# Optimization experiments

Hardware: AMD Instinct MI355X
Metric: run time of the kernel (lower is better)

## Reference

```python
import jax, jax.numpy as jnp
import numpy as np
from jax import lax

B, L, D_MODEL = 2, 1024, 768
N_LAYER, D_STATE, D_CONV, EXPAND = 8, 16, 4, 2
D_INNER = EXPAND * D_MODEL          # 1536
DT_RANK = -(-D_MODEL // 16)         # 48 (MambaConfig 'auto')


def setup_inputs() -> dict:
    key = jax.random.key(0)
    ks = jax.random.split(key, 10)
    s = 0.02
    batch = jax.random.normal(ks[0], (B, D_MODEL, L), jnp.float32)
    lengths = jax.random.randint(ks[1], (B,), L // 2, L + 1)
    mask = jnp.arange(L)[None, :] < lengths[:, None]          # valid-prefix mask [B,L]
    norm_w = jnp.ones((N_LAYER, D_MODEL), jnp.float32)
    W_in = jax.random.normal(ks[2], (N_LAYER, 2 * D_INNER, D_MODEL), jnp.float32) * s
    conv_w = jax.random.normal(ks[3], (N_LAYER, D_INNER, D_CONV), jnp.float32) * 0.5
    conv_b = jnp.zeros((N_LAYER, D_INNER), jnp.float32)
    W_x = jax.random.normal(ks[4], (N_LAYER, DT_RANK + 2 * D_STATE, D_INNER), jnp.float32) * s
    W_dt = jax.random.normal(ks[5], (N_LAYER, D_INNER, DT_RANK), jnp.float32) * (DT_RANK ** -0.5)
    # mamba dt init: dt ~ logU[1e-3, 0.1], bias = softplus^-1(dt)
    dt = jnp.exp(jax.random.uniform(ks[6], (N_LAYER, D_INNER)) * (np.log(0.1) - np.log(1e-3)) + np.log(1e-3))
    b_dt = jnp.log(jnp.expm1(dt)).astype(jnp.float32)
    A_log = jnp.log(jnp.broadcast_to(jnp.arange(1, D_STATE + 1, dtype=jnp.float32), (N_LAYER, D_INNER, D_STATE))).copy()
    D_skip = jnp.ones((N_LAYER, D_INNER), jnp.float32)
    W_out = jax.random.normal(ks[7], (N_LAYER, D_MODEL, D_INNER), jnp.float32) * s
    normf_w = jnp.ones((D_MODEL,), jnp.float32)
    return dict(batch=batch, mask=mask, norm_w=norm_w, W_in=W_in, conv_w=conv_w, conv_b=conv_b,
                W_x=W_x, W_dt=W_dt, b_dt=b_dt, A_log=A_log, D_skip=D_skip, W_out=W_out, normf_w=normf_w)


def _rmsnorm(x, w, eps=1e-5):
    return x * w * lax.rsqrt(jnp.mean(x * x, axis=-1, keepdims=True) + eps)


def _mamba(x, W_in, cw, cb, W_x, W_dt, b_dt, A_log, Dsk, W_out):
    Bb, Ls, _ = x.shape
    d_inner, d_conv = cw.shape
    d_state = A_log.shape[-1]
    dt_rank = W_dt.shape[-1]
    xz = jnp.einsum('bld,ed->ble', x, W_in)                    # [B,L,2*d_inner]
    xc, z = jnp.split(xz, 2, axis=-1)
    # causal depthwise conv1d (+bias) then SiLU
    xt = lax.conv_general_dilated(xc.transpose(0, 2, 1), cw[:, None, :], (1,),
                                  [(d_conv - 1, 0)], feature_group_count=d_inner)
    u = jax.nn.silu(xt + cb[None, :, None]).transpose(0, 2, 1)  # [B,L,d_inner]
    dbl = jnp.einsum('bld,ed->ble', u, W_x)
    dtp, Bm, Cm = jnp.split(dbl, [dt_rank, dt_rank + d_state], axis=-1)
    delta = jax.nn.softplus(jnp.einsum('blr,dr->bld', dtp, W_dt) + b_dt)  # [B,L,d_inner]
    A = -jnp.exp(A_log)                                         # [d_inner,d_state]

    def step(h, t):
        d_t, b_t, c_t, u_t = t                                  # [B,di],[B,ds],[B,ds],[B,di]
        h = jnp.exp(d_t[..., None] * A) * h + (d_t * u_t)[..., None] * b_t[:, None, :]
        return h, jnp.einsum('bds,bs->bd', h, c_t)

    h0 = jnp.zeros((Bb, d_inner, d_state), x.dtype)
    _, ys = lax.scan(step, h0, (delta.transpose(1, 0, 2), Bm.transpose(1, 0, 2),
                                Cm.transpose(1, 0, 2), u.transpose(1, 0, 2)))
    y = ys.transpose(1, 0, 2) + u * Dsk
    return jnp.einsum('bld,ed->ble', y * jax.nn.silu(z), W_out)


def _forward(batch, mask, norm_w, W_in, conv_w, conv_b, W_x, W_dt, b_dt, A_log, D_skip, W_out, normf_w):
    h = jnp.transpose(batch, (0, 2, 1))                         # [B,L,D]
    for i in range(norm_w.shape[0]):                            # pre-norm residual blocks
        h = h + _mamba(_rmsnorm(h, norm_w[i]), W_in[i], conv_w[i], conv_b[i],
                       W_x[i], W_dt[i], b_dt[i], A_log[i], D_skip[i], W_out[i])
    h = _rmsnorm(h, normf_w)
    # last valid token: first False of mask (or L if none), minus 1
    inv = ~mask
    lengths = jnp.where(jnp.any(inv, axis=1), jnp.argmax(inv, axis=1), mask.shape[1]) - 1
    return jnp.take_along_axis(h, lengths[:, None, None], axis=1)[:, 0, :]


def reference(batch, mask, norm_w, W_in, conv_w, conv_b, W_x, W_dt, b_dt, A_log, D_skip, W_out, normf_w):
    return _forward(batch, mask, norm_w, W_in, conv_w, conv_b, W_x, W_dt, b_dt, A_log, D_skip, W_out, normf_w)
```

## Files before the change

### kernel.cpp

```cpp
#include <hip/hip_runtime.h>
#include <hip/hip_bf16.h>
#include <math.h>

#define BB 2
#define LL 1024
#define DM 768
#define NL 8
#define DS 16
#define DC 4
#define DI 1536
#define DTR 48
#define NTOK (BB*LL)
#define WXROWS (DTR + 2*DS)
#define NC 64
#define CT (LL/NC)
#define SKS 8
#define SKC (DI/SKS)
#define SK4 3
#define SK4C (DI/SK4)
#define DTB 8
#define RBLK 128

typedef __attribute__((ext_vector_type(8))) short bf16x8;
typedef __attribute__((ext_vector_type(4))) float f32x4;

__device__ inline void gload_lds16(const void* g, void* l) {
    __builtin_amdgcn_global_load_lds(
        (const __attribute__((address_space(1))) unsigned int*)g,
        (__attribute__((address_space(3))) unsigned int*)l, 16, 0, 0);
}

__device__ inline int xcd_swz(int orig, int nwg) {
    return (orig & 7) * (nwg >> 3) + (orig >> 3);
}

__device__ inline void gemm_core64(
    const __hip_bfloat16* __restrict__ gA0,
    const __hip_bfloat16* __restrict__ gW0, const __hip_bfloat16* __restrict__ gW1,
    int kbeg, int kend, int w, int wr, int wc, int fr, int khi,
    f32x4 (&acc)[2][4])
{
    __shared__ short As[2048];
    __shared__ short Ws[4096];
    short* AsW = As + w * 512;
    short* WsW = Ws + w * 512;
    for (int k0 = kbeg; k0 < kend; k0 += 32) {
        gload_lds16(gA0 + k0, AsW);
        gload_lds16(gW0 + k0, WsW);
        gload_lds16(gW1 + k0, WsW + 2048);
        asm volatile("s_waitcnt vmcnt(0)" ::: "memory");
        __syncthreads();
        bf16x8 a4[2], b4[4];
        #pragma unroll
        for (int mi = 0; mi < 2; ++mi)
            a4[mi] = *(const bf16x8*)&As[(wr*32 + mi*16 + fr)*32 + khi*8];
        #pragma unroll
        for (int ni = 0; ni < 4; ++ni)
            b4[ni] = *(const bf16x8*)&Ws[(wc*64 + ni*16 + fr)*32 + khi*8];
        #pragma unroll
        for (int mi = 0; mi < 2; ++mi)
            #pragma unroll
            for (int ni = 0; ni < 4; ++ni)
                acc[mi][ni] = __builtin_amdgcn_mfma_f32_16x16x32_bf16(
                    a4[mi], b4[ni], acc[mi][ni], 0, 0, 0);
        __syncthreads();
    }
}

__global__ __launch_bounds__(256) void transpose_in_kernel(
    const float* __restrict__ batch, float* __restrict__ h)
{
    __shared__ float tile[32][33];
    const int b  = blockIdx.z;
    const int l0 = blockIdx.x * 32;
    const int d0 = blockIdx.y * 32;
    const int tx = threadIdx.x & 31;
    const int ty = threadIdx.x >> 5;
    #pragma unroll
    for (int i = ty; i < 32; i += 8)
        tile[i][tx] = batch[((size_t)b*DM + d0 + i)*LL + l0 + tx];
    __syncthreads();
    #pragma unroll
    for (int i = ty; i < 32; i += 8)
        h[((size_t)b*LL + l0 + i)*DM + d0 + tx] = tile[tx][i];
}

__global__ void lengths_kernel(const void* __restrict__ mask, int* __restrict__ lengths)
{
    int b = threadIdx.x;
    if (b >= BB) return;
    const unsigned int* mi = (const unsigned int*)mask;
    bool packed = (mi[0] == 0x01010101u);
    int cnt = 0;
    if (packed) {
        const unsigned char* mb = (const unsigned char*)mask;
        for (int i = 0; i < LL; ++i) cnt += (mb[(size_t)b*LL + i] != 0);
    } else {
        for (int i = 0; i < LL; ++i) cnt += (mi[(size_t)b*LL + i] != 0);
    }
    lengths[b] = cnt;
}

__global__ __launch_bounds__(256) void cvt_bf16_kernel(
    const float* __restrict__ in, __hip_bfloat16* __restrict__ o, int n)
{
    int i = (blockIdx.x * 256 + threadIdx.x) * 4;
    if (i >= n) return;
    float4 v = *(const float4*)(in + i);
    __hip_bfloat16 h0 = __float2bfloat16(v.x);
    __hip_bfloat16 h1 = __float2bfloat16(v.y);
    __hip_bfloat16 h2 = __float2bfloat16(v.z);
    __hip_bfloat16 h3 = __float2bfloat16(v.w);
    ushort4 r;
    r.x = *(unsigned short*)&h0; r.y = *(unsigned short*)&h1;
    r.z = *(unsigned short*)&h2; r.w = *(unsigned short*)&h3;
    *(ushort4*)(o + i) = r;
}

__global__ __launch_bounds__(256) void cvt_padrow_kernel(
    const float* __restrict__ in, __hip_bfloat16* __restrict__ o,
    int nrin, int nrout, int ncol, int nmat)
{
    int i = (blockIdx.x * 256 + threadIdx.x) * 4;
    int tot = nmat * nrout * ncol;
    if (i >= tot) return;
    int m = i / (nrout * ncol);
    int rem = i - m * (nrout * ncol);
    int r = rem / ncol;
    int c = rem - r * ncol;
    ushort4 rr = {0,0,0,0};
    if (r < nrin) {
        float4 v = *(const float4*)(in + ((size_t)m*nrin + r)*ncol + c);
        __hip_bfloat16 h0 = __float2bfloat16(v.x);
        __hip_bfloat16 h1 = __float2bfloat16(v.y);
        __hip_bfloat16 h2 = __float2bfloat16(v.z);
        __hip_bfloat16 h3 = __float2bfloat16(v.w);
        rr.x = *(unsigned short*)&h0; rr.y = *(unsigned short*)&h1;
        rr.z = *(unsigned short*)&h2; rr.w = *(unsigned short*)&h3;
    }
    *(ushort4*)(o + i) = rr;
}

__global__ __launch_bounds__(256) void rmsnorm_kernel(
    const float* __restrict__ x, const float* __restrict__ w,
    __hip_bfloat16* __restrict__ o)
{
    int tok = blockIdx.x;
    const float* xr = x + (size_t)tok * DM;
    float ss = 0.f;
    for (int j = threadIdx.x; j < DM; j += 256) { float v = xr[j]; ss += v*v; }
    #pragma unroll
    for (int off = 32; off > 0; off >>= 1) ss += __shfl_down(ss, off);
    __shared__ float red[4];
    int lane = threadIdx.x & 63, wv = threadIdx.x >> 6;
    if (lane == 0) red[wv] = ss;
    __syncthreads();
    if (threadIdx.x == 0) {
        float t = red[0] + red[1] + red[2] + red[3];
        red[0] = rsqrtf(t / (float)DM + 1e-5f);
    }
    __syncthreads();
    float r = red[0];
    for (int j = threadIdx.x; j < DM; j += 256)
        o[(size_t)tok*DM + j] = __float2bfloat16(xr[j] * w[j] * r);
}

__global__ __launch_bounds__(256) void gemm_mfma_kernel(
    const __hip_bfloat16* __restrict__ A,
    const __hip_bfloat16* __restrict__ W,
    __hip_bfloat16* __restrict__ C,
    int NT, int M, int N, int K)
{
    const int swz = xcd_swz(blockIdx.x, gridDim.x);
    const int bn = (swz % NT) * 128;
    const int bm = (swz / NT) * 64;
    const int t = threadIdx.x;
    const int w = t >> 6;
    const int lane = t & 63;
    const int wr = w >> 1, wc = w & 1;
    const int fr = lane & 15;
    const int khi = lane >> 4;

    f32x4 acc[2][4];
    #pragma unroll
    for (int mi = 0; mi < 2; ++mi)
        #pragma unroll
        for (int ni = 0; ni < 4; ++ni)
            acc[mi][ni] = (f32x4){0.f, 0.f, 0.f, 0.f};

    const int rowL = t >> 2;
    const int ks = (t & 3) * 8;
    gemm_core64(A + (size_t)(bm + rowL) * K + ks,
                W + (size_t)(bn + rowL) * K + ks,
                W + (size_t)(bn + 64 + rowL) * K + ks,
                0, K, w, wr, wc, fr, khi, acc);

    #pragma unroll
    for (int mi = 0; mi < 2; ++mi) {
        #pragma unroll
        for (int ni = 0; ni < 4; ++ni) {
            int gc = bn + wc*64 + ni*16 + fr;
            #pragma unroll
            for (int r = 0; r < 4; ++r) {
                int gr = bm + wr*32 + mi*16 + khi*4 + r;
                C[(size_t)gr * N + gc] = __float2bfloat16(acc[mi][ni][r]);
            }
        }
    }
}

__global__ __launch_bounds__(256) void gemm_mfma_splitk4(
    const __hip_bfloat16* __restrict__ A,
    const __hip_bfloat16* __restrict__ W,
    float* __restrict__ Cp)
{
    const int swz = xcd_swz(blockIdx.x, gridDim.x);
    const int bm = (swz / 18) * 64;
    const int r18 = swz % 18;
    const int bn = (r18 % 6) * 128;
    const int split = r18 / 6;
    const int t = threadIdx.x;
    const int w = t >> 6;
    const int lane = t & 63;
    const int wr = w >> 1, wc = w & 1;
    const int fr = lane & 15;
    const int khi = lane >> 4;

    f32x4 acc[2][4];
    #pragma unroll
    for (int mi = 0; mi < 2; ++mi)
        #pragma unroll
        for (int ni = 0; ni < 4; ++ni)
            acc[mi][ni] = (f32x4){0.f, 0.f, 0.f, 0.f};

    const int rowL = t >> 2;
    const int ks = (t & 3) * 8;
    const int kbeg = split * SK4C;
    gemm_core64(A + (size_t)(bm + rowL) * DI + ks,
                W + (size_t)(bn + rowL) * DI + ks,
                W + (size_t)(bn + 64 + rowL) * DI + ks,
                kbeg, kbeg + SK4C, w, wr, wc, fr, khi, acc);

    #pragma unroll
    for (int mi = 0; mi < 2; ++mi) {
        #pragma unroll
        for (int ni = 0; ni < 4; ++ni) {
            int gc = bn + wc*64 + ni*16 + fr;
            #pragma unroll
            for (int r = 0; r < 4; ++r) {
                int gr = bm + wr*32 + mi*16 + khi*4 + r;
                Cp[((size_t)split*NTOK + gr)*DM + gc] = acc[mi][ni][r];
            }
        }
    }
}

__global__ __launch_bounds__(256) void reduce_add_norm_kernel(
    const float* __restrict__ Cp, float* __restrict__ h,
    const float* __restrict__ nw, __hip_bfloat16* __restrict__ xn)
{
    int tok = blockIdx.x;
    int tid = threadIdx.x;
    float v[3];
    float ss = 0.f;
    #pragma unroll
    for (int r = 0; r < 3; ++r) {
        int j = tid + r*256;
        size_t o = (size_t)tok*DM + j;
        float x = h[o] + Cp[o] + Cp[(size_t)NTOK*DM + o] + Cp[2*(size_t)NTOK*DM + o];
        h[o] = x;
        v[r] = x;
        ss += x*x;
    }
    if (!nw) return;
    #pragma unroll
    for (int off = 32; off > 0; off >>= 1) ss += __shfl_down(ss, off);
    __shared__ float red[4];
    int lane = tid & 63, wv = tid >> 6;
    if (lane == 0) red[wv] = ss;
    __syncthreads();
    if (tid == 0) {
        float t = red[0] + red[1] + red[2] + red[3];
        red[0] = rsqrtf(t / (float)DM + 1e-5f);
    }
    __syncthreads();
    float rinv = red[0];
    #pragma unroll
    for (int r = 0; r < 3; ++r) {
        int j = tid + r*256;
        xn[(size_t)tok*DM + j] = __float2bfloat16(v[r] * nw[j] * rinv);
    }
}

__global__ __launch_bounds__(256) void gemm_mfma_skinny(
    const __hip_bfloat16* __restrict__ A,
    const __hip_bfloat16* __restrict__ W,
    float* __restrict__ Cp)
{
    const int split = blockIdx.x;
    const int bm = blockIdx.y * 64;
    const int t = threadIdx.x;
    const int w = t >> 6;
    const int lane = t & 63;
    const int wr = w >> 1, wc = w & 1;
    const int fr = lane & 15;
    const int khi = lane >> 4;

    f32x4 acc[2][4];
    #pragma unroll
    for (int mi = 0; mi < 2; ++mi)
        #pragma unroll
        for (int ni = 0; ni < 4; ++ni)
            acc[mi][ni] = (f32x4){0.f, 0.f, 0.f, 0.f};

    const int rowL = t >> 2;
    const int ks = (t & 3) * 8;
    const int kbeg = split * SKC;
    gemm_core64(A + (size_t)(bm + rowL) * DI + ks,
                W + (size_t)rowL * DI + ks,
                W + (size_t)(64 + rowL) * DI + ks,
                kbeg, kbeg + SKC, w, wr, wc, fr, khi, acc);

    #pragma unroll
    for (int mi = 0; mi < 2; ++mi) {
        #pragma unroll
        for (int ni = 0; ni < 4; ++ni) {
            int gc = wc*64 + ni*16 + fr;
            if (gc >= WXROWS) continue;
            #pragma unroll
            for (int r = 0; r < 4; ++r) {
                int gr = bm + wr*32 + mi*16 + khi*4 + r;
                Cp[((size_t)split*NTOK + gr)*WXROWS + gc] = acc[mi][ni][r];
            }
        }
    }
}

__global__ __launch_bounds__(256) void reduce_delta_kernel(
    const float* __restrict__ Cp,
    const float* __restrict__ W_dt, const float* __restrict__ b_dt,
    float* __restrict__ dbl, __hip_bfloat16* __restrict__ delta)
{
    __shared__ float ld[DTB*DTR];
    const int tid = threadIdx.x;
    const int d = blockIdx.x * 256 + tid;
    const int t0 = blockIdx.y * DTB;
    for (int j = tid; j < DTB*DTR; j += 256) {
        int tt = j / DTR, jj = j - tt*DTR;
        float s = 0.f;
        #pragma unroll
        for (int p = 0; p < SKS; ++p)
            s += Cp[((size_t)p*NTOK + t0 + tt)*WXROWS + jj];
        ld[j] = s;
    }
    if (blockIdx.x == 0) {
        for (int j = tid; j < DTB*WXROWS; j += 256) {
            int tt = j / WXROWS, jj = j - tt*WXROWS;
            float s = 0.f;
            #pragma unroll
            for (int p = 0; p < SKS; ++p)
                s += Cp[((size_t)p*NTOK + t0 + tt)*WXROWS + jj];
            dbl[(size_t)(t0 + tt)*WXROWS + jj] = s;
        }
    }
    float wdt[DTR];
    #pragma unroll
    for (int j = 0; j < DTR; j += 4) {
        float4 v = *(const float4*)(W_dt + (size_t)d*DTR + j);
        wdt[j] = v.x; wdt[j+1] = v.y; wdt[j+2] = v.z; wdt[j+3] = v.w;
    }
    const float bdt = b_dt[d];
    __syncthreads();
    #pragma unroll
    for (int tt = 0; tt < DTB; ++tt) {
        float dt = bdt;
        #pragma unroll
        for (int j = 0; j < DTR; ++j) dt = fmaf(ld[tt*DTR + j], wdt[j], dt);
        dt = (dt > 20.f) ? dt : log1pf(__expf(dt));
        delta[(size_t)(t0 + tt)*DI + d] = __float2bfloat16(dt);
    }
}

__global__ __launch_bounds__(256) void conv_silu_kernel(
    const __hip_bfloat16* __restrict__ xz, const float* __restrict__ cw,
    const float* __restrict__ cb, __hip_bfloat16* __restrict__ u)
{
    int idx = blockIdx.x * 256 + threadIdx.x;
    if (idx >= NTOK*DI/8) return;
    const int dg  = idx % (DI/8);
    const int row = idx / (DI/8);
    const int l   = row % LL;
    const int d0  = dg * 8;

    float acc[8];
    {
        float4 c0 = *(const float4*)(cb + d0);
        float4 c1 = *(const float4*)(cb + d0 + 4);
        acc[0]=c0.x; acc[1]=c0.y; acc[2]=c0.z; acc[3]=c0.w;
        acc[4]=c1.x; acc[5]=c1.y; acc[6]=c1.z; acc[7]=c1.w;
    }
    float4 cwj[8];
    #pragma unroll
    for (int j = 0; j < 8; ++j)
        cwj[j] = *(const float4*)(cw + (size_t)(d0 + j)*4);

    #pragma unroll
    for (int k = 0; k < 4; ++k) {
        int ls = l - 3 + k;
        if (ls < 0) continue;
        bf16x8 v = *(const bf16x8*)(xz + (size_t)(row - 3 + k)*(2*DI) + d0);
        const __hip_bfloat16* vp = (const __hip_bfloat16*)&v;
        #pragma unroll
        for (int j = 0; j < 8; ++j) {
            float xv = __bfloat162float(vp[j]);
            float wv = (k == 0) ? cwj[j].x : (k == 1) ? cwj[j].y : (k == 2) ? cwj[j].z : cwj[j].w;
            acc[j] = fmaf(xv, wv, acc[j]);
        }
    }
    bf16x8 r;
    __hip_bfloat16* rp = (__hip_bfloat16*)&r;
    #pragma unroll
    for (int j = 0; j < 8; ++j) {
        float s = acc[j] / (1.f + __expf(-acc[j]));
        rp[j] = __float2bfloat16(s);
    }
    *(bf16x8*)(u + (size_t)row*DI + d0) = r;
}

__global__ __launch_bounds__(256) void scan_phaseA(
    const __hip_bfloat16* __restrict__ delta, const __hip_bfloat16* __restrict__ u,
    const float* __restrict__ dbl, const float* __restrict__ A_log,
    __hip_bfloat16* __restrict__ Psum, __hip_bfloat16* __restrict__ Hsum)
{
    const int d = blockIdx.x * 256 + threadIdx.x;
    const int c = blockIdx.y;
    const int b = blockIdx.z;
    float A[DS], P[DS], hl[DS];
    #pragma unroll
    for (int s = 0; s < DS; ++s) {
        A[s] = -expf(A_log[(size_t)d*DS + s]);
        P[s] = 1.f; hl[s] = 0.f;
    }
    const int t0 = c * CT;
    for (int t = t0; t < t0 + CT; ++t) {
        const size_t row = (size_t)b*LL + t;
        const float* bc = dbl + row*WXROWS + DTR;
        float dt = __bfloat162float(delta[row*DI + d]);
        float du = dt * __bfloat162float(u[row*DI + d]);
        #pragma unroll
        for (int s = 0; s < DS; ++s) {
            float a = __expf(dt * A[s]);
            P[s] *= a;
            hl[s] = fmaf(a, hl[s], du * bc[s]);
        }
    }
    const size_t off = (((size_t)b*NC + c)*DI + d)*DS;
    #pragma unroll
    for (int s = 0; s < DS; ++s) {
        Psum[off+s] = __float2bfloat16(P[s]);
        Hsum[off+s] = __float2bfloat16(hl[s]);
    }
}

__global__ __launch_bounds__(256) void scan_phaseB(
    const __hip_bfloat16* __restrict__ Psum, const __hip_bfloat16* __restrict__ Hsum,
    __hip_bfloat16* __restrict__ Hin)
{
    __shared__ float pA[NC][RBLK];
    __shared__ float hA[NC][RBLK];
    const int tid = threadIdx.x;
    const int blk = blockIdx.x;
    const int b = blk / (DI*DS/RBLK);
    const int r0 = (blk % (DI*DS/RBLK)) * RBLK;
    for (int j = tid; j < NC*RBLK; j += 256) {
        int c = j >> 7, rr = j & (RBLK-1);
        size_t off = ((size_t)(b*NC + c))*DI*DS + r0 + rr;
        pA[c][rr] = __bfloat162float(Psum[off]);
        hA[c][rr] = __bfloat162float(Hsum[off]);
    }
    __syncthreads();
    if (tid < RBLK) {
        float hc = 0.f;
        for (int c = 0; c < NC; ++c) {
            size_t off = ((size_t)(b*NC + c))*DI*DS + r0 + tid;
            Hin[off] = __float2bfloat16(hc);
            hc = fmaf(pA[c][tid], hc, hA[c][tid]);
        }
    }
}

__global__ __launch_bounds__(256) void scan_phaseC(
    const __hip_bfloat16* __restrict__ delta, const __hip_bfloat16* __restrict__ u,
    const float* __restrict__ dbl, const __hip_bfloat16* __restrict__ xz,
    const float* __restrict__ A_log, const float* __restrict__ Dsk,
    const __hip_bfloat16* __restrict__ Hin, __hip_bfloat16* __restrict__ yfull)
{
    const int d = blockIdx.x * 256 + threadIdx.x;
    const int c = blockIdx.y;
    const int b = blockIdx.z;
    float A[DS], h[DS];
    const size_t hoff = (((size_t)b*NC + c)*DI + d)*DS;
    #pragma unroll
    for (int s = 0; s < DS; ++s) {
        A[s] = -expf(A_log[(size_t)d*DS + s]);
        h[s] = __bfloat162float(Hin[hoff + s]);
    }
    const float dsk = Dsk[d];
    const int t0 = c * CT;
    for (int t = t0; t < t0 + CT; ++t) {
        const size_t row = (size_t)b*LL + t;
        const float* bc = dbl + row*WXROWS + DTR;
        float dt = __bfloat162float(delta[row*DI + d]);
        float ut = __bfloat162float(u[row*DI + d]);
        float du = dt * ut;
        float y = 0.f;
        #pragma unroll
        for (int s = 0; s < DS; ++s) {
            float a = __expf(dt * A[s]);
            h[s] = fmaf(a, h[s], du * bc[s]);
            y = fmaf(h[s], bc[DS+s], y);
        }
        float zt = __bfloat162float(xz[row*(2*DI) + DI + d]);
        float sz = zt / (1.f + __expf(-zt));
        yfull[row*DI + d] = __float2bfloat16((y + ut * dsk) * sz);
    }
}

__global__ __launch_bounds__(256) void final_kernel(
    const float* __restrict__ h, const float* __restrict__ w,
    const int* __restrict__ lengths, float* __restrict__ out)
{
    int b = blockIdx.x;
    int idx = lengths[b] - 1;
    const float* xr = h + ((size_t)b*LL + idx)*DM;
    float ss = 0.f;
    for (int j = threadIdx.x; j < DM; j += 256) { float v = xr[j]; ss += v*v; }
    #pragma unroll
    for (int off = 32; off > 0; off >>= 1) ss += __shfl_down(ss, off);
    __shared__ float red[4];
    int lane = threadIdx.x & 63, wv = threadIdx.x >> 6;
    if (lane == 0) red[wv] = ss;
    __syncthreads();
    if (threadIdx.x == 0) {
        float t = red[0] + red[1] + red[2] + red[3];
        red[0] = rsqrtf(t / (float)DM + 1e-5f);
    }
    __syncthreads();
    float r = red[0];
    for (int j = threadIdx.x; j < DM; j += 256)
        out[(size_t)b*DM + j] = xr[j] * w[j] * r;
}

extern "C" void kernel_launch(void* const* d_in, const int* in_sizes, int n_in,
                              void* d_out, int out_size, void* d_ws, size_t ws_size,
                              hipStream_t stream)
{
    const float* batch   = (const float*)d_in[0];
    const void*  mask    = d_in[1];
    const float* norm_w  = (const float*)d_in[2];
    const float* W_in    = (const float*)d_in[3];
    const float* conv_w  = (const float*)d_in[4];
    const float* conv_b  = (const float*)d_in[5];
    const float* W_x     = (const float*)d_in[6];
    const float* W_dt    = (const float*)d_in[7];
    const float* b_dt    = (const float*)d_in[8];
    const float* A_log   = (const float*)d_in[9];
    const float* D_skip  = (const float*)d_in[10];
    const float* W_out   = (const float*)d_in[11];
    const float* normf_w = (const float*)d_in[12];
    float* out = (float*)d_out;

    float* ws   = (float*)d_ws;
    float* h    = ws;
    float* dbl  = h   + (size_t)NTOK*DM;
    float* scr  = dbl + (size_t)NTOK*WXROWS;
    const size_t SEG = (size_t)BB*NC*DI*DS;
    float* dblp = scr;
    float* Cp4  = scr;
    __hip_bfloat16* Psum = (__hip_bfloat16*)scr;
    __hip_bfloat16* Hsum = Psum + SEG;
    __hip_bfloat16* Hin  = Hsum + SEG;
    __hip_bfloat16* xz_bf    = (__hip_bfloat16*)(scr + 3*SEG);
    __hip_bfloat16* xn_bf    = xz_bf + (size_t)NTOK*2*DI;
    __hip_bfloat16* u_bf     = xn_bf + (size_t)NTOK*DM;
    __hip_bfloat16* delta_bf = u_bf  + (size_t)NTOK*DI;
    __hip_bfloat16* y_bf     = delta_bf + (size_t)NTOK*DI;
    __hip_bfloat16* wbase    = y_bf + (size_t)NTOK*DI;

    const size_t WIN_L  = (size_t)2*DI*DM;
    const size_t WOUT_L = (size_t)DM*DI;
    const size_t WXP_L  = (size_t)128*DI;
    const size_t WSUM   = WIN_L + WOUT_L + WXP_L;

    size_t need_all = (size_t)((char*)(wbase + (size_t)NL*WSUM) - (char*)d_ws) + 256;
    const bool all = ws_size >= need_all;
    const int nlw = all ? NL : 1;

    __hip_bfloat16* Win_b  = wbase;
    __hip_bfloat16* Wout_b = Win_b  + (size_t)nlw*WIN_L;
    __hip_bfloat16* Wxp_b  = Wout_b + (size_t)nlw*WOUT_L;
    int* lengths = (int*)(Wxp_b + (size_t)nlw*WXP_L);

    transpose_in_kernel<<<dim3(LL/32, DM/32, BB), 256, 0, stream>>>(batch, h);
    lengths_kernel<<<1, 64, 0, stream>>>(mask, lengths);

    if (all) {
        cvt_bf16_kernel<<<(int)(NL*WIN_L/4/256), 256, 0, stream>>>(W_in, Win_b, (int)(NL*WIN_L));
        cvt_bf16_kernel<<<(int)(NL*WOUT_L/4/256), 256, 0, stream>>>(W_out, Wout_b, (int)(NL*WOUT_L));
        cvt_padrow_kernel<<<(int)(NL*WXP_L/4/256), 256, 0, stream>>>(
            W_x, Wxp_b, WXROWS, 128, DI, NL);
    }

    rmsnorm_kernel<<<NTOK, 256, 0, stream>>>(h, norm_w, xn_bf);

    for (int i = 0; i < NL; ++i) {
        const float* cwi  = conv_w + (size_t)i * DI * DC;
        const float* cbi  = conv_b + (size_t)i * DI;
        const float* Wdti = W_dt  + (size_t)i * DI * DTR;
        const float* bdti = b_dt  + (size_t)i * DI;
        const float* Ali  = A_log + (size_t)i * DI * DS;
        const float* Dski = D_skip + (size_t)i * DI;

        if (!all) {
            cvt_bf16_kernel<<<(int)(WIN_L/4/256), 256, 0, stream>>>(
                W_in + (size_t)i*WIN_L, Win_b, (int)WIN_L);
            cvt_bf16_kernel<<<(int)(WOUT_L/4/256), 256, 0, stream>>>(
                W_out + (size_t)i*WOUT_L, Wout_b, (int)WOUT_L);
            cvt_padrow_kernel<<<(int)(WXP_L/4/256), 256, 0, stream>>>(
                W_x + (size_t)i*WXROWS*DI, Wxp_b, WXROWS, 128, DI, 1);
        }
        const __hip_bfloat16* Win_l  = Win_b  + (all ? (size_t)i*WIN_L  : 0);
        const __hip_bfloat16* Wout_l = Wout_b + (all ? (size_t)i*WOUT_L : 0);
        const __hip_bfloat16* Wxp_l  = Wxp_b  + (all ? (size_t)i*WXP_L  : 0);

        gemm_mfma_kernel<<<(2*DI/128)*(NTOK/64), 256, 0, stream>>>(
            xn_bf, Win_l, xz_bf, 2*DI/128, NTOK, 2*DI, DM);
        conv_silu_kernel<<<(NTOK*DI/8 + 255)/256, 256, 0, stream>>>(xz_bf, cwi, cbi, u_bf);
        gemm_mfma_skinny<<<dim3(SKS, NTOK/64), 256, 0, stream>>>(u_bf, Wxp_l, dblp);
        reduce_delta_kernel<<<dim3(DI/256, NTOK/DTB), 256, 0, stream>>>(
            dblp, Wdti, bdti, dbl, delta_bf);
        scan_phaseA<<<dim3(DI/256, NC, BB), 256, 0, stream>>>(
            delta_bf, u_bf, dbl, Ali, Psum, Hsum);
        scan_phaseB<<<BB*DI*DS/RBLK, 256, 0, stream>>>(Psum, Hsum, Hin);
        scan_phaseC<<<dim3(DI/256, NC, BB), 256, 0, stream>>>(
            delta_bf, u_bf, dbl, xz_bf, Ali, Dski, Hin, y_bf);
        gemm_mfma_splitk4<<<SK4*(NTOK/64)*(DM/128), 256, 0, stream>>>(
            y_bf, Wout_l, Cp4);
        reduce_add_norm_kernel<<<NTOK, 256, 0, stream>>>(
            Cp4, h, (i < NL-1) ? (norm_w + (size_t)(i+1)*DM) : nullptr, xn_bf);
    }

    final_kernel<<<BB, 256, 0, stream>>>(h, normf_w, lengths, out);
}
```

Baseline: 1.064 ms.

## Double scan chunk count, unroll scan loops, and process two K-slices per GEMM barrier

Raises the number of scan chunks from 64 to 128, which halves the tokens per chunk and doubles parallelism in the scan phase A and C kernels; phase B's block width shrinks to match. The phase A and C time loops are now fully unrolled. The GEMM core loads two 32-wide K slices per iteration into double LDS buffers, so there are half as many barriers and wait points. The bf16 scratch layout is recomputed to reflect that the segments are bf16, which also frees workspace. The cost is a longer sequential carry in phase B and larger Psum/Hsum traffic.

```diff
diff --git a/kernel.cpp b/kernel.cpp
--- a/kernel.cpp
+++ b/kernel.cpp
@@ -12,14 +12,14 @@
 #define DTR 48
 #define NTOK (BB*LL)
 #define WXROWS (DTR + 2*DS)
-#define NC 64
+#define NC 128
 #define CT (LL/NC)
 #define SKS 8
 #define SKC (DI/SKS)
 #define SK4 3
 #define SK4C (DI/SK4)
 #define DTB 8
-#define RBLK 128
+#define RBLK 64
 
 typedef __attribute__((ext_vector_type(8))) short bf16x8;
 typedef __attribute__((ext_vector_type(4))) float f32x4;
@@ -40,29 +40,33 @@
     int kbeg, int kend, int w, int wr, int wc, int fr, int khi,
     f32x4 (&acc)[2][4])
 {
-    __shared__ short As[2048];
-    __shared__ short Ws[4096];
-    short* AsW = As + w * 512;
-    short* WsW = Ws + w * 512;
-    for (int k0 = kbeg; k0 < kend; k0 += 32) {
-        gload_lds16(gA0 + k0, AsW);
-        gload_lds16(gW0 + k0, WsW);
-        gload_lds16(gW1 + k0, WsW + 2048);
+    __shared__ short As[2][2048];
+    __shared__ short Ws[2][4096];
+    for (int k0 = kbeg; k0 < kend; k0 += 64) {
+        gload_lds16(gA0 + k0,      &As[0][w*512]);
+        gload_lds16(gA0 + k0 + 32, &As[1][w*512]);
+        gload_lds16(gW0 + k0,      &Ws[0][w*512]);
+        gload_lds16(gW0 + k0 + 32, &Ws[1][w*512]);
+        gload_lds16(gW1 + k0,      &Ws[0][w*512 + 2048]);
+        gload_lds16(gW1 + k0 + 32, &Ws[1][w*512 + 2048]);
         asm volatile("s_waitcnt vmcnt(0)" ::: "memory");
         __syncthreads();
-        bf16x8 a4[2], b4[4];
-        #pragma unroll
-        for (int mi = 0; mi < 2; ++mi)
-            a4[mi] = *(const bf16x8*)&As[(wr*32 + mi*16 + fr)*32 + khi*8];
-        #pragma unroll
-        for (int ni = 0; ni < 4; ++ni)
-            b4[ni] = *(const bf16x8*)&Ws[(wc*64 + ni*16 + fr)*32 + khi*8];
-        #pragma unroll
-        for (int mi = 0; mi < 2; ++mi)
+        #pragma unroll
+        for (int kk = 0; kk < 2; ++kk) {
+            bf16x8 a4[2], b4[4];
+            #pragma unroll
+            for (int mi = 0; mi < 2; ++mi)
+                a4[mi] = *(const bf16x8*)&As[kk][(wr*32 + mi*16 + fr)*32 + khi*8];
             #pragma unroll
             for (int ni = 0; ni < 4; ++ni)
-                acc[mi][ni] = __builtin_amdgcn_mfma_f32_16x16x32_bf16(
-                    a4[mi], b4[ni], acc[mi][ni], 0, 0, 0);
+                b4[ni] = *(const bf16x8*)&Ws[kk][(wc*64 + ni*16 + fr)*32 + khi*8];
+            #pragma unroll
+            for (int mi = 0; mi < 2; ++mi)
+                #pragma unroll
+                for (int ni = 0; ni < 4; ++ni)
+                    acc[mi][ni] = __builtin_amdgcn_mfma_f32_16x16x32_bf16(
+                        a4[mi], b4[ni], acc[mi][ni], 0, 0, 0);
+        }
         __syncthreads();
     }
 }
@@ -442,8 +446,9 @@
         P[s] = 1.f; hl[s] = 0.f;
     }
     const int t0 = c * CT;
-    for (int t = t0; t < t0 + CT; ++t) {
-        const size_t row = (size_t)b*LL + t;
+    #pragma unroll
+    for (int t = 0; t < CT; ++t) {
+        const size_t row = (size_t)b*LL + t0 + t;
         const float* bc = dbl + row*WXROWS + DTR;
         float dt = __bfloat162float(delta[row*DI + d]);
         float du = dt * __bfloat162float(u[row*DI + d]);
@@ -473,7 +478,7 @@
     const int b = blk / (DI*DS/RBLK);
     const int r0 = (blk % (DI*DS/RBLK)) * RBLK;
     for (int j = tid; j < NC*RBLK; j += 256) {
-        int c = j >> 7, rr = j & (RBLK-1);
+        int c = j >> 6, rr = j & (RBLK-1);
         size_t off = ((size_t)(b*NC + c))*DI*DS + r0 + rr;
         pA[c][rr] = __bfloat162float(Psum[off]);
         hA[c][rr] = __bfloat162float(Hsum[off]);
@@ -507,8 +512,9 @@
     }
     const float dsk = Dsk[d];
     const int t0 = c * CT;
-    for (int t = t0; t < t0 + CT; ++t) {
-        const size_t row = (size_t)b*LL + t;
+    #pragma unroll
+    for (int t = 0; t < CT; ++t) {
+        const size_t row = (size_t)b*LL + t0 + t;
         const float* bc = dbl + row*WXROWS + DTR;
         float dt = __bfloat162float(delta[row*DI + d]);
         float ut = __bfloat162float(u[row*DI + d]);
@@ -574,13 +580,13 @@
     float* h    = ws;
     float* dbl  = h   + (size_t)NTOK*DM;
     float* scr  = dbl + (size_t)NTOK*WXROWS;
-    const size_t SEG = (size_t)BB*NC*DI*DS;
+    const size_t SEGB = (size_t)BB*NC*DI*DS;
     float* dblp = scr;
     float* Cp4  = scr;
     __hip_bfloat16* Psum = (__hip_bfloat16*)scr;
-    __hip_bfloat16* Hsum = Psum + SEG;
-    __hip_bfloat16* Hin  = Hsum + SEG;
-    __hip_bfloat16* xz_bf    = (__hip_bfloat16*)(scr + 3*SEG);
+    __hip_bfloat16* Hsum = Psum + SEGB;
+    __hip_bfloat16* Hin  = Hsum + SEGB;
+    __hip_bfloat16* xz_bf    = (__hip_bfloat16*)(scr + 3*SEGB/2);
     __hip_bfloat16* xn_bf    = xz_bf + (size_t)NTOK*2*DI;
     __hip_bfloat16* u_bf     = xn_bf + (size_t)NTOK*DM;
     __hip_bfloat16* delta_bf = u_bf  + (size_t)NTOK*DI;
```

After: 1.061 ms. No clear change (-0.3%).
